# Performance work log

Hardware: AMD Instinct MI355X
Metric: run time of the kernel (lower is better)

Reference implementation:

```python
import jax, jax.numpy as jnp
import numpy as np

B_SZ, L, H, D, N, R, K = 2, 1024, 2048, 4096, 16, 128, 4


def setup_inputs() -> dict:
    key = jax.random.key(0)
    ks = jax.random.split(key, 10)
    s = lambda *sh: 1.0 / np.sqrt(sh[-1])
    inp = {
        "hidden_states": jax.random.normal(ks[0], (B_SZ, L, H), jnp.float32),
        "in_proj_w": jax.random.normal(ks[1], (2 * D, H), jnp.float32) * s(H),
        "conv_w": jax.random.normal(ks[2], (D, 1, K), jnp.float32) * s(K),
        "conv_b": jax.random.normal(ks[3], (D,), jnp.float32) * 0.02,
        "x_proj_w": jax.random.normal(ks[4], (R + 2 * N, D), jnp.float32) * s(D),
        "dt_proj_w": jax.random.normal(ks[5], (D, R), jnp.float32) * s(R),
        "dt_proj_b": jax.random.normal(ks[6], (D,), jnp.float32) * 0.02,
        # A_log = log(arange(1, N+1)) broadcast over D, as in the module init
        "A_log": jnp.broadcast_to(jnp.log(jnp.arange(1, N + 1, dtype=jnp.float32))[None, :], (D, N)),
        "D_param": jnp.ones((D,), jnp.float32),
        "out_proj_w": jax.random.normal(ks[7], (H, D), jnp.float32) * s(D),
    }
    return inp


def _mamba_forward(hidden_states, in_proj_w, conv_w, conv_b, x_proj_w,
                   dt_proj_w, dt_proj_b, A_log, D_param, out_proj_w):
    silu = jax.nn.silu
    # in_proj: [B,L,H] @ [H,2D] -> [B,L,2D] -> [B,2D,L]
    proj = jnp.einsum("blh,ph->bpl", hidden_states, in_proj_w)
    u, gate = jnp.split(proj, 2, axis=1)  # each [B,D,L]
    # depthwise causal conv1d (padding K-1 on the left, then first L outputs)
    u = jax.lax.conv_general_dilated(
        u, conv_w, window_strides=(1,), padding=[(K - 1, 0)],
        dimension_numbers=("NCH", "OIH", "NCH"), feature_group_count=D,
    ) + conv_b[None, :, None]
    u = silu(u)  # [B,D,L]
    # x_proj on [B,L,D]
    ssm_params = jnp.einsum("bdl,pd->blp", u, x_proj_w)  # [B,L,R+2N]
    time_step, Bmat, Cmat = jnp.split(ssm_params, [R, R + N], axis=-1)
    # dt_proj + softplus -> [B,D,L]
    dt = jnp.einsum("blr,dr->bld", time_step, dt_proj_w) + dt_proj_b
    dt = jax.nn.softplus(dt).transpose(0, 2, 1)  # [B,D,L]
    A = -jnp.exp(A_log)  # [D,N]

    # selective scan over time; carry ssm_state [B,D,N]
    def step(state, xs):
        dt_t, B_t, C_t, u_t = xs  # [B,D],[B,N],[B,N],[B,D]
        dA = jnp.exp(A[None] * dt_t[:, :, None])          # [B,D,N]
        dBu = dt_t[:, :, None] * B_t[:, None, :] * u_t[:, :, None]
        state = dA * state + dBu
        y_t = jnp.einsum("bdn,bn->bd", state, C_t)        # [B,D]
        return state, y_t

    xs = (dt.transpose(2, 0, 1),          # [L,B,D]
          Bmat.transpose(1, 0, 2),        # [L,B,N]
          Cmat.transpose(1, 0, 2),        # [L,B,N]
          u.transpose(2, 0, 1))           # [L,B,D]
    init = jnp.zeros((hidden_states.shape[0], D, N), hidden_states.dtype)
    _, ys = jax.lax.scan(step, init, xs)   # ys [L,B,D]
    y = ys.transpose(1, 2, 0)              # [B,D,L]
    y = y + u * D_param[None, :, None]
    y = y * silu(gate)
    # out_proj: [B,L,D] @ [D,H]
    return jnp.einsum("bdl,hd->blh", y, out_proj_w)


def reference(hidden_states, in_proj_w, conv_w, conv_b, x_proj_w,
              dt_proj_w, dt_proj_b, A_log, D_param, out_proj_w):
    return _mamba_forward(hidden_states, in_proj_w, conv_w, conv_b, x_proj_w,
                          dt_proj_w, dt_proj_b, A_log, D_param, out_proj_w)
```

## Files before the change

kernel.cpp:

```cpp
#include <hip/hip_runtime.h>

#define L_SEQ 1024
#define DD 4096
#define NC 32
#define CT 32

typedef short bf16x8 __attribute__((ext_vector_type(8)));
typedef float f32x4 __attribute__((ext_vector_type(4)));
typedef unsigned short u16;

typedef const __attribute__((address_space(1))) void gas_t;
typedef __attribute__((address_space(3))) void las_t;

__device__ inline u16 f2bf(float f) {
  unsigned int u = __float_as_uint(f);
  u = (u + 0x7FFFu + ((u >> 16) & 1u)) >> 16;
  return (u16)u;
}

__device__ inline float bf2f(u16 v) {
  return __uint_as_float(((unsigned int)v) << 16);
}

__device__ inline float softplusf(float x) {
  return x > 20.f ? x : log1pf(expf(x));
}

__global__ __launch_bounds__(256) void cast_all_k(
    const float* __restrict__ hs, const float* __restrict__ w_in,
    const float* __restrict__ xw, const float* __restrict__ dtw,
    const float* __restrict__ ow, u16* __restrict__ hs_bf,
    u16* __restrict__ win_bf, u16* __restrict__ xw_bf,
    u16* __restrict__ dtw_bf, u16* __restrict__ ow_bf) {
  const int blk = blockIdx.x;
  const float* s;
  u16* d;
  int base;
  if (blk < 4096)        { s = hs;   d = hs_bf;  base = blk; }
  else if (blk < 20480)  { s = w_in; d = win_bf; base = blk - 4096; }
  else if (blk < 21120)  { s = xw;   d = xw_bf;  base = blk - 20480; }
  else if (blk < 21632)  { s = dtw;  d = dtw_bf; base = blk - 21120; }
  else                   { s = ow;   d = ow_bf;  base = blk - 21632; }
  const int i = (base * 256 + threadIdx.x) * 4;
  float4 v = *(const float4*)(s + i);
  ushort4 o;
  o.x = f2bf(v.x); o.y = f2bf(v.y); o.z = f2bf(v.z); o.w = f2bf(v.w);
  *(ushort4*)(d + i) = o;
}

__global__ __launch_bounds__(256) void reduce4b_k(const u16* __restrict__ p,
                                                  float* __restrict__ out,
                                                  long n) {
  long i = ((long)blockIdx.x * 256 + threadIdx.x) * 8;
  if (i >= n) return;
  uint4 a = *(const uint4*)(p + i);
  uint4 b = *(const uint4*)(p + n + i);
  uint4 c = *(const uint4*)(p + 2 * n + i);
  uint4 d = *(const uint4*)(p + 3 * n + i);
  const u16* qa = (const u16*)&a;
  const u16* qb = (const u16*)&b;
  const u16* qc = (const u16*)&c;
  const u16* qd = (const u16*)&d;
  float o[8];
#pragma unroll
  for (int j = 0; j < 8; j++)
    o[j] = (bf2f(qa[j]) + bf2f(qb[j])) + (bf2f(qc[j]) + bf2f(qd[j]));
  *(float4*)(out + i) = make_float4(o[0], o[1], o[2], o[3]);
  *(float4*)(out + i + 4) = make_float4(o[4], o[5], o[6], o[7]);
}

__global__ __launch_bounds__(256) void xproj_fin_k(const float* __restrict__ parts,
                                                   u16* __restrict__ ts,
                                                   float* __restrict__ ssm) {
  const int idx = blockIdx.x * 256 + threadIdx.x;
  float s = 0.f;
#pragma unroll
  for (int z = 0; z < 16; z++) s += parts[z * 327680 + idx];
  const int row = idx / 160;
  const int col = idx - row * 160;
  if (col < 128) ts[row * 128 + col] = f2bf(s);
  else ssm[idx] = s;
}

template <int CMODE, bool SWZ>
__global__ __launch_bounds__(512, 2) void gemm256(const u16* __restrict__ A,
                                                  const u16* __restrict__ B,
                                                  void* __restrict__ Cv,
                                                  int Nld, int K, int kc,
                                                  long zstride) {
  __shared__ u16 lds[3][2][8192];
  const int tid = threadIdx.x;
  const int lane = tid & 63, wid = tid >> 6;
  const int wm = wid >> 2, wn = wid & 3;
  int ty = blockIdx.y, tx = blockIdx.x;
  if (SWZ) {
    int flat = blockIdx.y * 32 + blockIdx.x;
    int xcd = flat & 7, pos = flat >> 3;
    ty = (xcd & 1) * 4 + (pos >> 3);
    tx = (xcd >> 1) * 8 + (pos & 7);
  }
  const long tm = (long)ty * 256, tn = (long)tx * 256;

  const long ks0 = (CMODE == 2) ? (long)blockIdx.z * kc : 0;

  const int srow = tid >> 2;
  const int sks = (((tid & 3) ^ ((srow >> 1) & 3))) * 8;
  const u16* gA0 = A + (tm + srow) * (long)K + ks0 + sks;
  const u16* gA1 = A + (tm + 128 + srow) * (long)K + ks0 + sks;
  const u16* gB0 = B + (tn + srow) * (long)K + ks0 + sks;
  const u16* gB1 = B + (tn + 128 + srow) * (long)K + ks0 + sks;
  const int sb0 = wid * 512;
  const int sb1 = 4096 + wid * 512;

  f32x4 acc[8][4] = {};

  const int lr = lane & 15, kq = lane >> 4;
  const int arow = wm * 128 + lr;
  const int brow = wn * 64 + lr;
  const int granA = (kq ^ ((arow >> 1) & 3)) * 8;
  const int granB = (kq ^ ((brow >> 1) & 3)) * 8;

  const int KT = kc >> 5;

#define STG1(b, k, c)                                                          \
  {                                                                            \
    const long ko_ = (long)(k) << 5;                                           \
    if ((c) == 0)                                                              \
      __builtin_amdgcn_global_load_lds((gas_t*)(gA0 + ko_),                    \
                                       (las_t*)&lds[b][0][sb0], 16, 0, 0);     \
    else if ((c) == 1)                                                         \
      __builtin_amdgcn_global_load_lds((gas_t*)(gA1 + ko_),                    \
                                       (las_t*)&lds[b][0][sb1], 16, 0, 0);     \
    else if ((c) == 2)                                                         \
      __builtin_amdgcn_global_load_lds((gas_t*)(gB0 + ko_),                    \
                                       (las_t*)&lds[b][1][sb0], 16, 0, 0);     \
    else                                                                       \
      __builtin_amdgcn_global_load_lds((gas_t*)(gB1 + ko_),                    \
                                       (las_t*)&lds[b][1][sb1], 16, 0, 0);     \
  }

  STG1(0, 0, 0); STG1(0, 0, 1); STG1(0, 0, 2); STG1(0, 0, 3);
  if (KT > 1) { STG1(1, 1, 0); STG1(1, 1, 1); STG1(1, 1, 2); STG1(1, 1, 3); }

  int buf = 0;
  for (int kt = 0; kt < KT; ++kt) {
    if (kt + 1 < KT)
      asm volatile("s_waitcnt vmcnt(4)" ::: "memory");
    else
      asm volatile("s_waitcnt vmcnt(0)" ::: "memory");
    __builtin_amdgcn_s_barrier();

    const int nb = (buf == 0) ? 2 : buf - 1;
    const bool doS = (kt + 2) < KT;
    bf16x8 bfr[4];
#pragma unroll
    for (int p = 0; p < 4; ++p) {
      bf16x8 a0 = *(const bf16x8*)&lds[buf][0][(arow + (2 * p) * 16) * 32 + granA];
      bf16x8 a1 = *(const bf16x8*)&lds[buf][0][(arow + (2 * p + 1) * 16) * 32 + granA];
      if (p == 0) {
#pragma unroll
        for (int n = 0; n < 4; n++)
          bfr[n] = *(const bf16x8*)&lds[buf][1][(brow + n * 16) * 32 + granB];
      }
      if (doS) STG1(nb, kt + 2, p);
      asm volatile("s_waitcnt lgkmcnt(0)" ::: "memory");
      __builtin_amdgcn_s_setprio(1);
#pragma unroll
      for (int n = 0; n < 4; n++)
        acc[2 * p][n] = __builtin_amdgcn_mfma_f32_16x16x32_bf16(
            a0, bfr[n], acc[2 * p][n], 0, 0, 0);
#pragma unroll
      for (int n = 0; n < 4; n++)
        acc[2 * p + 1][n] = __builtin_amdgcn_mfma_f32_16x16x32_bf16(
            a1, bfr[n], acc[2 * p + 1][n], 0, 0, 0);
      __builtin_amdgcn_s_setprio(0);
      __builtin_amdgcn_s_barrier();
    }
    buf = (buf == 2) ? 0 : buf + 1;
  }
#undef STG1

  const int rg = (lane >> 4) * 4;
#pragma unroll
  for (int m = 0; m < 8; m++) {
    const long gr = tm + wm * 128 + m * 16 + rg;
#pragma unroll
    for (int n = 0; n < 4; n++) {
      const long gc = tn + wn * 64 + n * 16 + lr;
#pragma unroll
      for (int r = 0; r < 4; r++) {
        if (CMODE == 1)
          ((u16*)Cv)[(gr + r) * (long)Nld + gc] = f2bf(acc[m][n][r]);
        else
          ((u16*)Cv)[(long)blockIdx.z * zstride + (gr + r) * (long)Nld + gc] =
              f2bf(acc[m][n][r]);
      }
    }
  }
}

template <bool CLAMP_N, int MODE>
__global__ __launch_bounds__(256) void gemm_bt(const u16* __restrict__ A,
                                               const u16* __restrict__ B,
                                               void* __restrict__ Cv,
                                               const float* __restrict__ ebias,
                                               int Nv, int K, int ldc, int kc,
                                               long zs) {
  __shared__ u16 lA[128 * 32];
  __shared__ u16 lB[128 * 32];
  const int tid = threadIdx.x;
  const int lane = tid & 63, wid = tid >> 6;
  const int wm = wid >> 1, wn = wid & 1;
  const long tm = (long)blockIdx.y * 128, tn = (long)blockIdx.x * 128;

  f32x4 acc[4][4] = {};

  const int roff = lane >> 2;
  const int sks = (((lane & 3) ^ ((roff >> 1) & 3))) * 8;
  const int c0 = wid * 2, c1 = c0 + 1;
  const long ra0 = tm + c0 * 16 + roff;
  const long ra1 = tm + c1 * 16 + roff;
  long rb0 = tn + c0 * 16 + roff;
  long rb1 = tn + c1 * 16 + roff;
  if (CLAMP_N) {
    if (rb0 >= Nv) rb0 = Nv - 1;
    if (rb1 >= Nv) rb1 = Nv - 1;
  }
  const u16* gA0 = A + ra0 * K + sks;
  const u16* gA1 = A + ra1 * K + sks;
  const u16* gB0 = B + rb0 * K + sks;
  const u16* gB1 = B + rb1 * K + sks;
  u16* sA0 = &lA[c0 * 512];
  u16* sA1 = &lA[c1 * 512];
  u16* sB0 = &lB[c0 * 512];
  u16* sB1 = &lB[c1 * 512];

  int ks0 = 0, ks1 = K;
  if (MODE == 2) { ks0 = blockIdx.z * kc; ks1 = ks0 + kc; }

  const int lr = lane & 15, kq = lane >> 4;
  const int arow = wm * 64 + lr, brow = wn * 64 + lr;
  const int granA = (kq ^ ((arow >> 1) & 3)) * 8;
  const int granB = (kq ^ ((brow >> 1) & 3)) * 8;

  for (int ks = ks0; ks < ks1; ks += 32) {
    __builtin_amdgcn_global_load_lds((gas_t*)(gA0 + ks), (las_t*)sA0, 16, 0, 0);
    __builtin_amdgcn_global_load_lds((gas_t*)(gA1 + ks), (las_t*)sA1, 16, 0, 0);
    __builtin_amdgcn_global_load_lds((gas_t*)(gB0 + ks), (las_t*)sB0, 16, 0, 0);
    __builtin_amdgcn_global_load_lds((gas_t*)(gB1 + ks), (las_t*)sB1, 16, 0, 0);
    __syncthreads();
    bf16x8 af[4], bfr[4];
#pragma unroll
    for (int i = 0; i < 4; i++) {
      af[i]  = *(const bf16x8*)&lA[(arow + i * 16) * 32 + granA];
      bfr[i] = *(const bf16x8*)&lB[(brow + i * 16) * 32 + granB];
    }
#pragma unroll
    for (int i = 0; i < 4; i++)
#pragma unroll
      for (int j = 0; j < 4; j++)
        acc[i][j] = __builtin_amdgcn_mfma_f32_16x16x32_bf16(af[i], bfr[j],
                                                            acc[i][j], 0, 0, 0);
    __syncthreads();
  }

  float* Cf = (MODE == 2) ? (float*)Cv + (long)blockIdx.z * zs : (float*)Cv;

  const int rg = (lane >> 4) * 4;
#pragma unroll
  for (int i = 0; i < 4; i++) {
    const long gr = tm + wm * 64 + i * 16 + rg;
#pragma unroll
    for (int j = 0; j < 4; j++) {
      const long gc = tn + wn * 64 + j * 16 + lr;
      if (CLAMP_N && gc >= Nv) continue;
      float bias = 0.f;
      if (MODE == 1) bias = ebias[gc];
#pragma unroll
      for (int r = 0; r < 4; r++) {
        float v = acc[i][j][r];
        if (MODE == 1)
          ((u16*)Cv)[(gr + r) * (long)ldc + gc] = f2bf(softplusf(v + bias));
        else
          Cf[(gr + r) * (long)ldc + gc] = v;
      }
    }
  }
}

__global__ __launch_bounds__(256) void conv_silu_k(const u16* __restrict__ projb,
                                                   const float* __restrict__ cw,
                                                   const float* __restrict__ cb,
                                                   u16* __restrict__ ub) {
  const int gid = blockIdx.x * 256 + threadIdx.x;
  const int d = (gid & 511) * 8;
  const int bl = gid >> 9;
  const int l = bl & (L_SEQ - 1);
  const u16* pp = projb + (long)bl * 8192 + d;
  const uint4 zero = make_uint4(0, 0, 0, 0);
  uint4 t0 = *(const uint4*)pp;
  uint4 t1 = (l >= 1) ? *(const uint4*)(pp - 8192) : zero;
  uint4 t2 = (l >= 2) ? *(const uint4*)(pp - 16384) : zero;
  uint4 t3 = (l >= 3) ? *(const uint4*)(pp - 24576) : zero;
  const u16* q0 = (const u16*)&t0;
  const u16* q1 = (const u16*)&t1;
  const u16* q2 = (const u16*)&t2;
  const u16* q3 = (const u16*)&t3;
  float4 b0 = *(const float4*)(cb + d);
  float4 b1 = *(const float4*)(cb + d + 4);
  u16 ov[8];
#pragma unroll
  for (int j = 0; j < 8; j++) {
    const float4 w = *(const float4*)(cw + (d + j) * 4);
    float s = (j < 4) ? ((const float*)&b0)[j] : ((const float*)&b1)[j - 4];
    s += w.w * bf2f(q0[j]);
    s += w.z * bf2f(q1[j]);
    s += w.y * bf2f(q2[j]);
    s += w.x * bf2f(q3[j]);
    const float r = s / (1.f + expf(-s));
    ov[j] = f2bf(r);
  }
  *(uint4*)(ub + (long)bl * DD + d) = *(uint4*)ov;
}

__global__ __launch_bounds__(256) void scan_p1(const u16* __restrict__ dt,
                                               const u16* __restrict__ u,
                                               const float* __restrict__ ssm,
                                               const float* __restrict__ A_log,
                                               float* __restrict__ Sbuf,
                                               float* __restrict__ Pbuf) {
  __shared__ float sBC[CT * 32];
  __shared__ u16 dtl[CT][256];
  __shared__ u16 ul[CT][256];
  const int tid = threadIdx.x;
  const int d0 = blockIdx.x * 256;
  const int d = d0 + tid;
  const int c = blockIdx.y, b = blockIdx.z;
  const long blbase = (long)b * L_SEQ + (long)c * CT;
  for (int i = tid; i < CT * 32; i += 256) {
    int tt = i >> 5, j = i & 31;
    sBC[i] = ssm[(blbase + tt) * 160 + 128 + j];
  }
  const u16* dtg = dt + blbase * DD + d0;
  const u16* ug  = u  + blbase * DD + d0;
#pragma unroll
  for (int it = 0; it < 4; ++it) {
    const int ck = it * 256 + tid;
    const int row = ck >> 5, ch = (ck & 31) * 8;
    *(uint4*)&dtl[row][ch] = *(const uint4*)(dtg + (long)row * DD + ch);
    *(uint4*)&ul[row][ch]  = *(const uint4*)(ug  + (long)row * DD + ch);
  }
  __syncthreads();
  float a2[16], st[16], pr[16];
#pragma unroll
  for (int g = 0; g < 4; g++) {
    float4 al = *(const float4*)(A_log + d * 16 + g * 4);
    a2[g*4+0] = -expf(al.x) * 1.4426950408889634f;
    a2[g*4+1] = -expf(al.y) * 1.4426950408889634f;
    a2[g*4+2] = -expf(al.z) * 1.4426950408889634f;
    a2[g*4+3] = -expf(al.w) * 1.4426950408889634f;
  }
#pragma unroll
  for (int n = 0; n < 16; n++) { st[n] = 0.f; pr[n] = 1.f; }
  for (int tt = 0; tt < CT; tt++) {
    const float dtv = bf2f(dtl[tt][tid]);
    const float uv = bf2f(ul[tt][tid]);
    const float dtu = dtv * uv;
    const float4* Bv = (const float4*)&sBC[tt * 32];
#pragma unroll
    for (int g = 0; g < 4; g++) {
      const float4 Bg = Bv[g];
      float e;
      e = exp2f(a2[g*4+0]*dtv); st[g*4+0] = e*st[g*4+0] + dtu*Bg.x; pr[g*4+0] *= e;
      e = exp2f(a2[g*4+1]*dtv); st[g*4+1] = e*st[g*4+1] + dtu*Bg.y; pr[g*4+1] *= e;
      e = exp2f(a2[g*4+2]*dtv); st[g*4+2] = e*st[g*4+2] + dtu*Bg.z; pr[g*4+2] *= e;
      e = exp2f(a2[g*4+3]*dtv); st[g*4+3] = e*st[g*4+3] + dtu*Bg.w; pr[g*4+3] *= e;
    }
  }
  const long base = (((long)b * NC + c) * DD + d) * 16;
#pragma unroll
  for (int g = 0; g < 4; g++) {
    *(float4*)(Sbuf + base + g * 4) = make_float4(st[g*4+0], st[g*4+1], st[g*4+2], st[g*4+3]);
    *(float4*)(Pbuf + base + g * 4) = make_float4(pr[g*4+0], pr[g*4+1], pr[g*4+2], pr[g*4+3]);
  }
}

__global__ __launch_bounds__(256) void scan_p2(const float* __restrict__ Sbuf,
                                               const float* __restrict__ Pbuf,
                                               float* __restrict__ carry) {
  const int idx = blockIdx.x * 256 + threadIdx.x;
  const int ng = idx & 3;
  const int d = (idx >> 2) & (DD - 1);
  const int b = idx >> 14;
  const long stride = (long)DD * 16;
  long base = ((long)b * NC * DD + d) * 16 + ng * 4;
  float4 P = *(const float4*)(Pbuf + base);
  float4 S = *(const float4*)(Sbuf + base);
  float4 cr = make_float4(0.f, 0.f, 0.f, 0.f);
  for (int c = 0; c < NC; c++) {
    float4 Pn, Sn;
    if (c + 1 < NC) {
      Pn = *(const float4*)(Pbuf + base + stride);
      Sn = *(const float4*)(Sbuf + base + stride);
    }
    *(float4*)(carry + base) = cr;
    cr.x = P.x * cr.x + S.x;
    cr.y = P.y * cr.y + S.y;
    cr.z = P.z * cr.z + S.z;
    cr.w = P.w * cr.w + S.w;
    P = Pn; S = Sn;
    base += stride;
  }
}

__global__ __launch_bounds__(256) void scan_p3(const u16* __restrict__ dt,
                                               const u16* __restrict__ u,
                                               const float* __restrict__ ssm,
                                               const u16* __restrict__ projb,
                                               const float* __restrict__ A_log,
                                               const float* __restrict__ Dp,
                                               const float* __restrict__ carry,
                                               u16* __restrict__ yb) {
  __shared__ float sBC[CT * 32];
  __shared__ u16 dtl[CT][256];
  __shared__ u16 ul[CT][256];
  const int tid = threadIdx.x;
  const int d0 = blockIdx.x * 256;
  const int d = d0 + tid;
  const int c = blockIdx.y, b = blockIdx.z;
  const long blbase = (long)b * L_SEQ + (long)c * CT;
  for (int i = tid; i < CT * 32; i += 256) {
    int tt = i >> 5, j = i & 31;
    sBC[i] = ssm[(blbase + tt) * 160 + 128 + j];
  }
  const u16* dtg = dt + blbase * DD + d0;
  const u16* ug  = u  + blbase * DD + d0;
#pragma unroll
  for (int it = 0; it < 4; ++it) {
    const int ck = it * 256 + tid;
    const int row = ck >> 5, ch = (ck & 31) * 8;
    *(uint4*)&dtl[row][ch] = *(const uint4*)(dtg + (long)row * DD + ch);
    *(uint4*)&ul[row][ch]  = *(const uint4*)(ug  + (long)row * DD + ch);
  }
  __syncthreads();
  float a2[16], st[16];
#pragma unroll
  for (int g = 0; g < 4; g++) {
    float4 al = *(const float4*)(A_log + d * 16 + g * 4);
    a2[g*4+0] = -expf(al.x) * 1.4426950408889634f;
    a2[g*4+1] = -expf(al.y) * 1.4426950408889634f;
    a2[g*4+2] = -expf(al.z) * 1.4426950408889634f;
    a2[g*4+3] = -expf(al.w) * 1.4426950408889634f;
  }
  const long cbase = (((long)b * NC + c) * DD + d) * 16;
#pragma unroll
  for (int g = 0; g < 4; g++) {
    float4 cv = *(const float4*)(carry + cbase + g * 4);
    st[g*4+0] = cv.x; st[g*4+1] = cv.y; st[g*4+2] = cv.z; st[g*4+3] = cv.w;
  }
  const float dp = Dp[d];
  const u16* gp = projb + blbase * 8192 + DD + d;
  u16 gnext = gp[0];
  for (int tt = 0; tt < CT; tt++) {
    const u16 gcur = gnext;
    if (tt + 1 < CT) gnext = gp[(tt + 1) * 8192];
    const float dtv = bf2f(dtl[tt][tid]);
    const float uv = bf2f(ul[tt][tid]);
    const float dtu = dtv * uv;
    float acc = 0.f;
    const float4* Bv = (const float4*)&sBC[tt * 32];
    const float4* Cv = Bv + 4;
#pragma unroll
    for (int g = 0; g < 4; g++) {
      const float4 Bg = Bv[g];
      const float4 Cg = Cv[g];
      float e;
      e = exp2f(a2[g*4+0]*dtv); st[g*4+0] = e*st[g*4+0] + dtu*Bg.x; acc += st[g*4+0]*Cg.x;
      e = exp2f(a2[g*4+1]*dtv); st[g*4+1] = e*st[g*4+1] + dtu*Bg.y; acc += st[g*4+1]*Cg.y;
      e = exp2f(a2[g*4+2]*dtv); st[g*4+2] = e*st[g*4+2] + dtu*Bg.z; acc += st[g*4+2]*Cg.z;
      e = exp2f(a2[g*4+3]*dtv); st[g*4+3] = e*st[g*4+3] + dtu*Bg.w; acc += st[g*4+3]*Cg.w;
    }
    const float g = bf2f(gcur);
    const float yv = (acc + uv * dp) * (g / (1.f + expf(-g)));
    yb[(blbase + tt) * DD + d] = f2bf(yv);
  }
}

extern "C" void kernel_launch(void* const* d_in, const int* in_sizes, int n_in,
                              void* d_out, int out_size, void* d_ws, size_t ws_size,
                              hipStream_t stream) {
  const float* hs     = (const float*)d_in[0];
  const float* w_in   = (const float*)d_in[1];
  const float* conv_w = (const float*)d_in[2];
  const float* conv_b = (const float*)d_in[3];
  const float* xw     = (const float*)d_in[4];
  const float* dtw    = (const float*)d_in[5];
  const float* dtb    = (const float*)d_in[6];
  const float* A_log  = (const float*)d_in[7];
  const float* Dp     = (const float*)d_in[8];
  const float* ow     = (const float*)d_in[9];
  float* out = (float*)d_out;

  constexpr size_t SZ_HS_BF  = 2048ull * 2048 * 2;
  constexpr size_t SZ_WIN_BF = 8192ull * 2048 * 2;
  constexpr size_t SZ_PROJ   = 2048ull * 8192 * 2;
  constexpr size_t SZ_UBF    = 2048ull * 4096 * 2;
  constexpr size_t SZ_XW_BF  = 160ull * 4096 * 2;
  constexpr size_t SZ_SSM    = 2048ull * 160 * 4;
  constexpr size_t SZ_TS_BF  = 2048ull * 128 * 2;
  constexpr size_t SZ_DTW_BF = 4096ull * 128 * 2;
  constexpr size_t SZ_DT     = 2048ull * 4096 * 2;
  constexpr size_t SZ_OW_BF  = 2048ull * 4096 * 2;
  constexpr size_t SZ_YBF    = 2048ull * 4096 * 2;
  constexpr size_t SZ_SCAN   = 2ull * NC * DD * 16 * 4;
  constexpr size_t TOTAL = SZ_HS_BF + SZ_WIN_BF + SZ_PROJ + SZ_UBF +
                           SZ_XW_BF + SZ_SSM + SZ_TS_BF + SZ_DTW_BF + SZ_DT +
                           SZ_OW_BF + SZ_YBF + 3 * SZ_SCAN;
  if (ws_size < TOTAL) return;

  char* w = (char*)d_ws;
  u16* hs_bf   = (u16*)w;   w += SZ_HS_BF;
  u16* win_bf  = (u16*)w;   w += SZ_WIN_BF;
  u16* projb   = (u16*)w;   w += SZ_PROJ;
  u16* u_bf    = (u16*)w;   w += SZ_UBF;
  u16* xw_bf   = (u16*)w;   w += SZ_XW_BF;
  float* ssm   = (float*)w; w += SZ_SSM;
  u16* ts_bf   = (u16*)w;   w += SZ_TS_BF;
  u16* dtw_bf  = (u16*)w;   w += SZ_DTW_BF;
  u16* dt_bf   = (u16*)w;   w += SZ_DT;
  u16* ow_bf   = (u16*)w;   w += SZ_OW_BF;
  u16* y_bf    = (u16*)w;   w += SZ_YBF;
  float* Sbuf  = (float*)w; w += SZ_SCAN;
  float* Pbuf  = (float*)w; w += SZ_SCAN;
  float* carry = (float*)w; w += SZ_SCAN;

  float* partsx = Sbuf;
  u16* parts = win_bf;

  cast_all_k<<<29824, 256, 0, stream>>>(hs, w_in, xw, dtw, ow,
                                        hs_bf, win_bf, xw_bf, dtw_bf, ow_bf);

  gemm256<1, true><<<dim3(32, 8), 512, 0, stream>>>(
      hs_bf, win_bf, projb, 8192, 2048, 2048, 0);

  conv_silu_k<<<4096, 256, 0, stream>>>(projb, conv_w, conv_b, u_bf);

  gemm_bt<true, 2><<<dim3(2, 16, 16), 256, 0, stream>>>(
      u_bf, xw_bf, partsx, nullptr, 160, 4096, 160, 256, 327680);

  xproj_fin_k<<<1280, 256, 0, stream>>>(partsx, ts_bf, ssm);

  gemm_bt<false, 1><<<dim3(32, 16), 256, 0, stream>>>(
      ts_bf, dtw_bf, dt_bf, dtb, 4096, 128, 4096, 0, 0);

  scan_p1<<<dim3(16, NC, 2), 256, 0, stream>>>(dt_bf, u_bf, ssm, A_log, Sbuf, Pbuf);
  scan_p2<<<128, 256, 0, stream>>>(Sbuf, Pbuf, carry);
  scan_p3<<<dim3(16, NC, 2), 256, 0, stream>>>(dt_bf, u_bf, ssm, projb, A_log, Dp,
                                               carry, y_bf);

  gemm256<2, false><<<dim3(8, 8, 4), 512, 0, stream>>>(
      y_bf, ow_bf, parts, 2048, 4096, 1024, 2048ll * 2048);
  reduce4b_k<<<2048, 256, 0, stream>>>(parts, out, 2048ll * 2048);
}
```

Baseline: 358.6 us.

## Switch GEMM to BK=64 double-buffered LDS pipeline with 8-way swizzle

Changes the 256x256 GEMM main loop from a triple-buffered 32-wide K step to a double-buffered 64-wide K step, with a matching 8-granule XOR swizzle and two MFMA K-halves per iteration. This halves the number of barrier/wait rounds per K and lengthens each compute phase between them. In exchange, LDS use per block grows to 128KB, occupancy is set to one block per CU, and the prefetch depth drops to a single stage with a full vmcnt(0) wait each iteration, which may expose load latency.

```diff
diff --git a/kernel.cpp b/kernel.cpp
--- a/kernel.cpp
+++ b/kernel.cpp
@@ -83,12 +83,12 @@
 }
 
 template <int CMODE, bool SWZ>
-__global__ __launch_bounds__(512, 2) void gemm256(const u16* __restrict__ A,
+__global__ __launch_bounds__(512, 1) void gemm256(const u16* __restrict__ A,
                                                   const u16* __restrict__ B,
                                                   void* __restrict__ Cv,
                                                   int Nld, int K, int kc,
                                                   long zstride) {
-  __shared__ u16 lds[3][2][8192];
+  __shared__ u16 lds[2][2][16384];
   const int tid = threadIdx.x;
   const int lane = tid & 63, wid = tid >> 6;
   const int wm = wid >> 2, wn = wid & 3;
@@ -103,82 +103,82 @@
 
   const long ks0 = (CMODE == 2) ? (long)blockIdx.z * kc : 0;
 
-  const int srow = tid >> 2;
-  const int sks = (((tid & 3) ^ ((srow >> 1) & 3))) * 8;
-  const u16* gA0 = A + (tm + srow) * (long)K + ks0 + sks;
-  const u16* gA1 = A + (tm + 128 + srow) * (long)K + ks0 + sks;
-  const u16* gB0 = B + (tn + srow) * (long)K + ks0 + sks;
-  const u16* gB1 = B + (tn + 128 + srow) * (long)K + ks0 + sks;
-  const int sb0 = wid * 512;
-  const int sb1 = 4096 + wid * 512;
+  const int srow = tid >> 3;
+  const int ssw = ((tid & 7) ^ ((srow >> 1) & 7)) * 8;
+  const u16* gA = A + (tm + srow) * (long)K + ks0 + ssw;
+  const u16* gB = B + (tn + srow) * (long)K + ks0 + ssw;
 
   f32x4 acc[8][4] = {};
 
   const int lr = lane & 15, kq = lane >> 4;
   const int arow = wm * 128 + lr;
   const int brow = wn * 64 + lr;
-  const int granA = (kq ^ ((arow >> 1) & 3)) * 8;
-  const int granB = (kq ^ ((brow >> 1) & 3)) * 8;
-
-  const int KT = kc >> 5;
-
-#define STG1(b, k, c)                                                          \
-  {                                                                            \
-    const long ko_ = (long)(k) << 5;                                           \
-    if ((c) == 0)                                                              \
-      __builtin_amdgcn_global_load_lds((gas_t*)(gA0 + ko_),                    \
-                                       (las_t*)&lds[b][0][sb0], 16, 0, 0);     \
-    else if ((c) == 1)                                                         \
-      __builtin_amdgcn_global_load_lds((gas_t*)(gA1 + ko_),                    \
-                                       (las_t*)&lds[b][0][sb1], 16, 0, 0);     \
-    else if ((c) == 2)                                                         \
-      __builtin_amdgcn_global_load_lds((gas_t*)(gB0 + ko_),                    \
-                                       (las_t*)&lds[b][1][sb0], 16, 0, 0);     \
-    else                                                                       \
-      __builtin_amdgcn_global_load_lds((gas_t*)(gB1 + ko_),                    \
-                                       (las_t*)&lds[b][1][sb1], 16, 0, 0);     \
-  }
-
-  STG1(0, 0, 0); STG1(0, 0, 1); STG1(0, 0, 2); STG1(0, 0, 3);
-  if (KT > 1) { STG1(1, 1, 0); STG1(1, 1, 1); STG1(1, 1, 2); STG1(1, 1, 3); }
-
-  int buf = 0;
-  for (int kt = 0; kt < KT; ++kt) {
-    if (kt + 1 < KT)
-      asm volatile("s_waitcnt vmcnt(4)" ::: "memory");
-    else
-      asm volatile("s_waitcnt vmcnt(0)" ::: "memory");
+  const int swA = (arow >> 1) & 7, swB = (brow >> 1) & 7;
+  const int granA0 = (kq ^ swA) * 8, granA1 = ((kq + 4) ^ swA) * 8;
+  const int granB0 = (kq ^ swB) * 8, granB1 = ((kq + 4) ^ swB) * 8;
+
+  const int KT = kc >> 6;
+
+#define STGA(bf_, s_, i_)                                                      \
+  __builtin_amdgcn_global_load_lds(                                            \
+      (gas_t*)(gA + (long)(i_) * 64 * K + ((long)(s_) << 6)),                  \
+      (las_t*)&lds[bf_][0][(i_) * 4096 + wid * 512], 16, 0, 0);
+#define STGB(bf_, s_, i_)                                                      \
+  __builtin_amdgcn_global_load_lds(                                            \
+      (gas_t*)(gB + (long)(i_) * 64 * K + ((long)(s_) << 6)),                  \
+      (las_t*)&lds[bf_][1][(i_) * 4096 + wid * 512], 16, 0, 0);
+
+  STGA(0, 0, 0); STGA(0, 0, 1); STGA(0, 0, 2); STGA(0, 0, 3);
+  STGB(0, 0, 0); STGB(0, 0, 1); STGB(0, 0, 2); STGB(0, 0, 3);
+
+  for (int s = 0; s < KT; ++s) {
+    asm volatile("s_waitcnt vmcnt(0)" ::: "memory");
     __builtin_amdgcn_s_barrier();
-
-    const int nb = (buf == 0) ? 2 : buf - 1;
-    const bool doS = (kt + 2) < KT;
-    bf16x8 bfr[4];
+    const int bf = s & 1, nb = bf ^ 1;
+    const bool doS = (s + 1) < KT;
+    bf16x8 bfr[4][2];
 #pragma unroll
     for (int p = 0; p < 4; ++p) {
-      bf16x8 a0 = *(const bf16x8*)&lds[buf][0][(arow + (2 * p) * 16) * 32 + granA];
-      bf16x8 a1 = *(const bf16x8*)&lds[buf][0][(arow + (2 * p + 1) * 16) * 32 + granA];
+      const int m0 = 2 * p, m1 = 2 * p + 1;
+      bf16x8 a00 = *(const bf16x8*)&lds[bf][0][(arow + m0 * 16) * 64 + granA0];
+      bf16x8 a01 = *(const bf16x8*)&lds[bf][0][(arow + m0 * 16) * 64 + granA1];
+      bf16x8 a10 = *(const bf16x8*)&lds[bf][0][(arow + m1 * 16) * 64 + granA0];
+      bf16x8 a11 = *(const bf16x8*)&lds[bf][0][(arow + m1 * 16) * 64 + granA1];
       if (p == 0) {
 #pragma unroll
-        for (int n = 0; n < 4; n++)
-          bfr[n] = *(const bf16x8*)&lds[buf][1][(brow + n * 16) * 32 + granB];
+        for (int n = 0; n < 4; n++) {
+          bfr[n][0] = *(const bf16x8*)&lds[bf][1][(brow + n * 16) * 64 + granB0];
+          bfr[n][1] = *(const bf16x8*)&lds[bf][1][(brow + n * 16) * 64 + granB1];
+        }
+        if (doS) { STGA(nb, s + 1, 0); STGA(nb, s + 1, 1);
+                   STGA(nb, s + 1, 2); STGA(nb, s + 1, 3); }
       }
-      if (doS) STG1(nb, kt + 2, p);
+      if (p == 1 && doS) { STGB(nb, s + 1, 0); STGB(nb, s + 1, 1);
+                           STGB(nb, s + 1, 2); STGB(nb, s + 1, 3); }
       asm volatile("s_waitcnt lgkmcnt(0)" ::: "memory");
       __builtin_amdgcn_s_setprio(1);
 #pragma unroll
       for (int n = 0; n < 4; n++)
-        acc[2 * p][n] = __builtin_amdgcn_mfma_f32_16x16x32_bf16(
-            a0, bfr[n], acc[2 * p][n], 0, 0, 0);
+        acc[m0][n] = __builtin_amdgcn_mfma_f32_16x16x32_bf16(a00, bfr[n][0],
+                                                             acc[m0][n], 0, 0, 0);
 #pragma unroll
       for (int n = 0; n < 4; n++)
-        acc[2 * p + 1][n] = __builtin_amdgcn_mfma_f32_16x16x32_bf16(
-            a1, bfr[n], acc[2 * p + 1][n], 0, 0, 0);
+        acc[m0][n] = __builtin_amdgcn_mfma_f32_16x16x32_bf16(a01, bfr[n][1],
+                                                             acc[m0][n], 0, 0, 0);
+#pragma unroll
+      for (int n = 0; n < 4; n++)
+        acc[m1][n] = __builtin_amdgcn_mfma_f32_16x16x32_bf16(a10, bfr[n][0],
+                                                             acc[m1][n], 0, 0, 0);
+#pragma unroll
+      for (int n = 0; n < 4; n++)
+        acc[m1][n] = __builtin_amdgcn_mfma_f32_16x16x32_bf16(a11, bfr[n][1],
+                                                             acc[m1][n], 0, 0, 0);
       __builtin_amdgcn_s_setprio(0);
       __builtin_amdgcn_s_barrier();
     }
-    buf = (buf == 2) ? 0 : buf + 1;
-  }
-#undef STG1
+  }
+#undef STGA
+#undef STGB
 
   const int rg = (lane >> 4) * 4;
 #pragma unroll
```

New measurement: 350.2 us. 1.02x faster.
